# Kernel optimization log

Measured on AMD Instinct MI355X. Metric: run time of the kernel, lower is better.

Reference implementation:

```python
import jax, jax.numpy as jnp
import numpy as np

F, N, H = 1024, 16, 64  # features, num_heads, head_dim
B, T, S = 2, 1024, 2048  # batch, query len, memory (kv) len
M = S + 1                # relative position embeddings length


def _relative_shift(x):
    # x: [B, N, T, M] -> [B, N, T, M-1]  (Transformer-XL relative shift)
    b, h, q_len, k_len = x.shape
    x = jnp.pad(x, ((0, 0), (0, 0), (0, 0), (1, 0)))
    x = x.reshape(b, h, k_len + 1, q_len)
    x = x[:, :, 1:, :]
    x = x.reshape(b, h, q_len, k_len)
    return x[..., :-1]


def setup_inputs() -> dict:
    key = jax.random.key(0)
    ks = jax.random.split(key, 12)
    s = 1.0 / np.sqrt(F)
    return {
        'x': jax.random.normal(ks[0], (B, T, F), jnp.float32),
        'rel': jax.random.normal(ks[1], (M, F), jnp.float32),
        'memory': jax.random.normal(ks[2], (B, S, F), jnp.float32),
        'Wq': jax.random.normal(ks[3], (F, N, H), jnp.float32) * s,
        'Wk': jax.random.normal(ks[4], (F, N, H), jnp.float32) * s,
        'Wv': jax.random.normal(ks[5], (F, N, H), jnp.float32) * s,
        'Wr': jax.random.normal(ks[6], (F, N, H), jnp.float32) * s,
        'u_bias': jnp.zeros((N, H), jnp.float32),
        'v_bias': jnp.zeros((N, H), jnp.float32),
        'Wout': jax.random.normal(ks[7], (N * H, F), jnp.float32) * (1.0 / np.sqrt(N * H)),
        'b_out': jnp.zeros((F,), jnp.float32),
    }


def reference(x, rel, memory, Wq, Wk, Wv, Wr, u_bias, v_bias, Wout, b_out):
    b, t = x.shape[0], x.shape[1]
    # projections (DenseGeneral, no bias)
    q = jnp.einsum('btf,fnh->btnh', x, Wq)
    k = jnp.einsum('bsf,fnh->bsnh', memory, Wk)
    v = jnp.einsum('bsf,fnh->bsnh', memory, Wv)
    r = jnp.einsum('mf,fnh->mnh', rel, Wr)
    head_dim = q.shape[-1]
    scale = 1.0 / jnp.sqrt(jnp.asarray(head_dim, jnp.float32))
    q_u = q + u_bias[None, None]
    q_v = q + v_bias[None, None]
    # relative position bias, materialized at [B,N,T,M] then shifted
    bd = jnp.einsum('btnh,mnh->bntm', q_v, r)
    bd = _relative_shift(bd)                        # [B,N,T,S]
    bias = (bd * scale).astype(jnp.float32)
    # attention (dot_product_attention math), q/k/v in bf16 per source
    qb = q_u.astype(jnp.bfloat16)
    kb = k.astype(jnp.bfloat16)
    vb = v.astype(jnp.bfloat16)
    logits = jnp.einsum('btnh,bsnh->bnts', qb, kb).astype(jnp.float32) * scale + bias
    probs = jax.nn.softmax(logits, axis=-1)         # fp32 softmax
    out = jnp.einsum('bnts,bsnh->btnh', probs.astype(jnp.bfloat16), vb)
    out = out.astype(jnp.float32).reshape(b, t, -1)  # [B,T,N*H]
    return out @ Wout + b_out
```

## Files before the change

kernel.cpp:

```cpp
#include <hip/hip_runtime.h>
#include <cmath>

#define C_SCALE 0.18033688011112042f

typedef __attribute__((ext_vector_type(8))) short bf16x8;
typedef __attribute__((ext_vector_type(8))) _Float16 half8;
typedef __attribute__((ext_vector_type(4))) _Float16 half4;
typedef __attribute__((ext_vector_type(4))) float f32x4;
typedef __attribute__((ext_vector_type(4))) unsigned short us4;

__device__ inline unsigned short bf16_rne(float f) {
    unsigned u = __builtin_bit_cast(unsigned, f);
    u += 0x7fff + ((u >> 16) & 1);
    return (unsigned short)(u >> 16);
}

__device__ inline void lds_dma16(const _Float16* g, _Float16* l) {
    __builtin_amdgcn_global_load_lds(
        (__attribute__((address_space(1))) void*)(void*)g,
        (__attribute__((address_space(3))) void*)(void*)l, 16, 0, 0);
}

__global__ __launch_bounds__(256) void prep_kernel(
    const float* __restrict__ x, const float* __restrict__ mem,
    const float* __restrict__ rel,
    const float* __restrict__ s0, const float* __restrict__ s1,
    const float* __restrict__ s2, const float* __restrict__ s3,
    const float* __restrict__ s4,
    _Float16* __restrict__ x16, _Float16* __restrict__ mem16,
    _Float16* __restrict__ rel16,
    _Float16* __restrict__ d0, _Float16* __restrict__ d1,
    _Float16* __restrict__ d2, _Float16* __restrict__ d3,
    _Float16* __restrict__ d4)
{
    const int bx = blockIdx.x, tid = threadIdx.x;
    if (bx < 1280) {
        __shared__ _Float16 T[64][72];
        const int z = bx >> 8, rem = bx & 255;
        const float* src = z == 0 ? s0 : z == 1 ? s1 : z == 2 ? s2 : z == 3 ? s3 : s4;
        _Float16*    dst = z == 0 ? d0 : z == 1 ? d1 : z == 2 ? d2 : z == 3 ? d3 : d4;
        const int r0 = (rem & 15) * 64, c0 = (rem >> 4) * 64;
        const int r = tid >> 4, c4 = (tid & 15) * 4;
        #pragma unroll
        for (int rr = 0; rr < 64; rr += 16) {
            float4 v = *(const float4*)(src + (size_t)(r0 + r + rr) * 1024 + c0 + c4);
            T[c4 + 0][r + rr] = (_Float16)v.x;
            T[c4 + 1][r + rr] = (_Float16)v.y;
            T[c4 + 2][r + rr] = (_Float16)v.z;
            T[c4 + 3][r + rr] = (_Float16)v.w;
        }
        __syncthreads();
        const int orow = tid >> 2, seg = (tid & 3) * 16;
        half8 h0 = *(const half8*)&T[orow][seg];
        half8 h1 = *(const half8*)&T[orow][seg + 8];
        *(half8*)(dst + (size_t)(c0 + orow) * 1024 + r0 + seg)     = h0;
        *(half8*)(dst + (size_t)(c0 + orow) * 1024 + r0 + seg + 8) = h1;
    } else {
        size_t i = ((size_t)(bx - 1280) * 256 + tid) * 8;
        if (i >= 8389632ull) return;
        const float* src; _Float16* dst; size_t off;
        if (i < 2097152ull)      { src = x;   dst = x16;   off = i; }
        else if (i < 6291456ull) { src = mem; dst = mem16; off = i - 2097152ull; }
        else                     { src = rel; dst = rel16; off = i - 6291456ull; }
        float4 a = *(const float4*)(src + off);
        float4 b = *(const float4*)(src + off + 4);
        half8 h;
        h[0]=(_Float16)a.x; h[1]=(_Float16)a.y; h[2]=(_Float16)a.z; h[3]=(_Float16)a.w;
        h[4]=(_Float16)b.x; h[5]=(_Float16)b.y; h[6]=(_Float16)b.z; h[7]=(_Float16)b.w;
        *(half8*)(dst + off) = h;
    }
}

__global__ __launch_bounds__(256) void proj3_kernel(
    const _Float16* __restrict__ x16, const _Float16* __restrict__ mem16,
    const _Float16* __restrict__ rel16,
    const _Float16* __restrict__ Wqt, const _Float16* __restrict__ Wkt,
    const _Float16* __restrict__ Wvt, const _Float16* __restrict__ Wrt,
    const float* __restrict__ ub, const float* __restrict__ vb,
    unsigned short* __restrict__ qu, _Float16* __restrict__ qv,
    unsigned short* __restrict__ kb, unsigned short* __restrict__ vtb,
    _Float16* __restrict__ rb)
{
    alignas(16) __shared__ _Float16 As[128 * 64];
    alignas(16) __shared__ _Float16 Bs[128 * 64];
    const int tid = threadIdx.x;
    const int lane = tid & 63, w = tid >> 6, c = lane & 15, g = lane >> 4;
    const int bx = blockIdx.x, col0 = blockIdx.y * 128;

    int mode, row0, rowmax;
    const _Float16 *Ap, *Bp;
    if (bx < 16)      { mode = 0; row0 = bx * 128;        rowmax = 2047; Ap = x16;   Bp = Wqt; }
    else if (bx < 48) { mode = 1; row0 = (bx - 16) * 128; rowmax = 4095; Ap = mem16; Bp = Wkt; }
    else if (bx < 80) { mode = 2; row0 = (bx - 48) * 128; rowmax = 4095; Ap = mem16; Bp = Wvt; }
    else              { mode = 3; row0 = (bx - 80) * 128; rowmax = 2048; Ap = rel16; Bp = Wrt; }

    const int qr = (w & 1) * 64, qc = (w >> 1) * 64;
    const int srow = lane >> 3, phys = lane & 7;
    f32x4 acc[4][4] = {};

    for (int k0 = 0; k0 < 1024; k0 += 64) {
        #pragma unroll
        for (int q = 0; q < 4; q++) {
            int row = 32 * w + 8 * q + srow;
            int log = phys ^ (row & 7);
            int ar = row0 + row; if (ar > rowmax) ar = rowmax;
            lds_dma16(Ap + (size_t)ar * 1024 + k0 + log * 8, &As[(32 * w + 8 * q) * 64]);
            lds_dma16(Bp + (size_t)(col0 + row) * 1024 + k0 + log * 8, &Bs[(32 * w + 8 * q) * 64]);
        }
        __syncthreads();
        #pragma unroll
        for (int s = 0; s < 2; s++) {
            half8 af[4], bf[4];
            #pragma unroll
            for (int i = 0; i < 4; i++) {
                int row = qr + 16 * i + c;
                af[i] = *(const half8*)&As[row * 64 + ((4 * s + g) ^ (row & 7)) * 8];
            }
            #pragma unroll
            for (int j = 0; j < 4; j++) {
                int row = qc + 16 * j + c;
                bf[j] = *(const half8*)&Bs[row * 64 + ((4 * s + g) ^ (row & 7)) * 8];
            }
            #pragma unroll
            for (int i = 0; i < 4; i++)
                #pragma unroll
                for (int j = 0; j < 4; j++)
                    acc[i][j] = __builtin_amdgcn_mfma_f32_16x16x32_f16(af[i], bf[j], acc[i][j], 0, 0, 0);
        }
        __syncthreads();
    }

    #pragma unroll
    for (int i = 0; i < 4; i++) {
        #pragma unroll
        for (int j = 0; j < 4; j++) {
            const int cg = col0 + qc + 16 * j + c;
            const int rbase = row0 + qr + 16 * i + 4 * g;
            if (mode == 0) {
                float u = ub[cg], v = vb[cg];
                #pragma unroll
                for (int rg = 0; rg < 4; rg++) {
                    size_t o = (size_t)(rbase + rg) * 1024 + cg;
                    qu[o] = bf16_rne(acc[i][j][rg] + u);
                    qv[o] = (_Float16)((acc[i][j][rg] + v) * C_SCALE);
                }
            } else if (mode == 1) {
                #pragma unroll
                for (int rg = 0; rg < 4; rg++)
                    kb[(size_t)(rbase + rg) * 1024 + cg] = bf16_rne(acc[i][j][rg]);
            } else if (mode == 2) {
                us4 pk;
                #pragma unroll
                for (int rg = 0; rg < 4; rg++) pk[rg] = bf16_rne(acc[i][j][rg]);
                int b = rbase >> 11, s = rbase & 2047;
                *(us4*)&vtb[((size_t)(b * 16 + (cg >> 6)) * 64 + (cg & 63)) * 2048 + s] = pk;
            } else {
                #pragma unroll
                for (int rg = 0; rg < 4; rg++) {
                    int r_g = rbase + rg;
                    if (r_g < 2049)
                        rb[((size_t)(cg >> 6) * 2049 + r_g) * 64 + (cg & 63)] = (_Float16)acc[i][j][rg];
                }
            }
        }
    }
}

__global__ __launch_bounds__(256) void flash_kernel(
    const unsigned short* __restrict__ qu, const _Float16* __restrict__ qv,
    const unsigned short* __restrict__ kg, const unsigned short* __restrict__ vt,
    const _Float16* __restrict__ rb, _Float16* __restrict__ po, float* __restrict__ pl)
{
    __shared__ unsigned short Ks[64 * 70];
    __shared__ unsigned short Vs[64 * 70];
    __shared__ unsigned short PsT[64 * 70];
    __shared__ _Float16 BDX[64 * 138];
    const int tid = threadIdx.x;
    const int lane = tid & 63, w = tid >> 6, c = lane & 15, g = lane >> 4;
    const int id = blockIdx.x;
    const int p_pair = id & 127;
    const int t0 = (id >> 7) * 64;
    const int bn = p_pair >> 2, part = p_pair & 3;
    const int b = bn >> 4, n = bn & 15;
    const int s_start = part * 512;
    const int d0 = s_start - t0;

    const int tg = t0 + 16 * w + c;
    const unsigned short* qp = qu + (size_t)(b * 1024 + tg) * 1024 + n * 64 + g * 8;
    bf16x8 qf0 = *(const bf16x8*)qp;
    bf16x8 qf1 = *(const bf16x8*)(qp + 32);
    const _Float16* qvp = qv + (size_t)(b * 1024 + tg) * 1024 + n * 64 + g * 8;
    half8 av0 = *(const half8*)qvp;
    half8 av1 = *(const half8*)(qvp + 32);
    int tg2 = tg + 1; if (tg2 > 1023) tg2 = 1023;
    const _Float16* qvp2 = qv + (size_t)(b * 1024 + tg2) * 1024 + n * 64 + g * 8;
    half8 aw0 = *(const half8*)qvp2;
    half8 aw1 = *(const half8*)(qvp2 + 32);

    const _Float16* rbase = rb + (size_t)n * 2049 * 64;

    f32x4 o[4] = {};
    float l_acc = 0.f;

    const int myrow = (16 * w + c);

    auto bd_quad = [&](int Dbase) {
        #pragma unroll
        for (int i = 0; i < 4; i++) {
            const int Dmin = Dbase + 16 * i;
            const int Drow = Dmin + c;
            int mm = (Drow <= 1026) ? (Drow + 1023 > 2048 ? 2048 : Drow + 1023)
                                    : Drow - 1027;
            const _Float16* rp = rbase + (size_t)mm * 64 + g * 8;
            half8 r0 = *(const half8*)rp;
            half8 r1 = *(const half8*)(rp + 32);
            f32x4 z;
            if (Dmin + 15 <= 1026) {
                f32x4 zm = {};
                zm = __builtin_amdgcn_mfma_f32_16x16x32_f16(r0, av0, zm, 0, 0, 0);
                zm = __builtin_amdgcn_mfma_f32_16x16x32_f16(r1, av1, zm, 0, 0, 0);
                z = zm;
            } else if (Dmin >= 1027) {
                f32x4 zw = {};
                zw = __builtin_amdgcn_mfma_f32_16x16x32_f16(r0, aw0, zw, 0, 0, 0);
                zw = __builtin_amdgcn_mfma_f32_16x16x32_f16(r1, aw1, zw, 0, 0, 0);
                z = zw;
            } else {
                f32x4 zm = {}, zw = {};
                zm = __builtin_amdgcn_mfma_f32_16x16x32_f16(r0, av0, zm, 0, 0, 0);
                zm = __builtin_amdgcn_mfma_f32_16x16x32_f16(r1, av1, zm, 0, 0, 0);
                zw = __builtin_amdgcn_mfma_f32_16x16x32_f16(r0, aw0, zw, 0, 0, 0);
                zw = __builtin_amdgcn_mfma_f32_16x16x32_f16(r1, aw1, zw, 0, 0, 0);
                #pragma unroll
                for (int rg = 0; rg < 4; rg++)
                    z[rg] = (Dmin + 4 * g + rg >= 1027) ? zw[rg] : zm[rg];
            }
            int dz = 1026 - Dmin - 4 * g;
            if (dz >= 0 && dz < 4) z[dz] = 0.f;
            half4 hv;
            #pragma unroll
            for (int rg = 0; rg < 4; rg++) hv[rg] = (_Float16)z[rg];
            int slot0 = (Dmin + 4 * g - d0 + 63) & 127;
            _Float16* wp = &BDX[myrow * 138 + slot0];
            *(half4*)wp = hv;
            if (slot0 < 4) *(half4*)(wp + 128) = hv;
        }
    };

    bd_quad(d0 - 63);
    bd_quad(d0 + 1);

    const int sr = tid >> 2, scc = (tid & 3) * 16;
    const unsigned short* kst = kg + (size_t)(b * 2048 + s_start + sr) * 1024 + n * 64 + scc;
    const unsigned short* vst = vt + ((size_t)bn * 64 + sr) * 2048 + s_start + scc;

    for (int kk = 0; kk < 8; kk++) {
        const int diff0 = d0 + kk * 64;

        *(uint4*)&Ks[sr * 70 + scc]     = *(const uint4*)(kst + (size_t)(kk * 64) * 1024);
        *(uint4*)&Ks[sr * 70 + scc + 8] = *(const uint4*)(kst + (size_t)(kk * 64) * 1024 + 8);
        *(uint4*)&Vs[sr * 70 + scc]     = *(const uint4*)(vst + kk * 64);
        *(uint4*)&Vs[sr * 70 + scc + 8] = *(const uint4*)(vst + kk * 64 + 8);
        __syncthreads();

        #pragma unroll
        for (int i = 0; i < 4; i++) {
            bf16x8 kf0 = *(const bf16x8*)&Ks[(16 * i + c) * 70 + 8 * g];
            bf16x8 kf1 = *(const bf16x8*)&Ks[(16 * i + c) * 70 + 32 + 8 * g];
            f32x4 sa = {};
            sa = __builtin_amdgcn_mfma_f32_16x16x32_bf16(kf0, qf0, sa, 0, 0, 0);
            sa = __builtin_amdgcn_mfma_f32_16x16x32_bf16(kf1, qf1, sa, 0, 0, 0);
            int slotb = (64 * kk + 16 * i + 4 * g - myrow + 63) & 127;
            half4 bd4 = *(const half4*)&BDX[myrow * 138 + slotb];
            us4 pk;
            #pragma unroll
            for (int rg = 0; rg < 4; rg++) {
                float p = exp2f(fmaf(sa[rg], C_SCALE, (float)bd4[rg]));
                l_acc += p;
                pk[rg] = bf16_rne(p);
            }
            *(us4*)&PsT[myrow * 70 + 16 * i + 4 * g] = pk;
        }

        if (kk < 7) bd_quad(diff0 + 65);

        bf16x8 pf0 = *(const bf16x8*)&PsT[myrow * 70 + 8 * g];
        bf16x8 pf1 = *(const bf16x8*)&PsT[myrow * 70 + 32 + 8 * g];
        #pragma unroll
        for (int i2 = 0; i2 < 4; i2++) {
            bf16x8 vf0 = *(const bf16x8*)&Vs[(16 * i2 + c) * 70 + 8 * g];
            bf16x8 vf1 = *(const bf16x8*)&Vs[(16 * i2 + c) * 70 + 32 + 8 * g];
            o[i2] = __builtin_amdgcn_mfma_f32_16x16x32_bf16(vf0, pf0, o[i2], 0, 0, 0);
            o[i2] = __builtin_amdgcn_mfma_f32_16x16x32_bf16(vf1, pf1, o[i2], 0, 0, 0);
        }
        __syncthreads();
    }

    float s2 = l_acc;
    s2 += __shfl_xor(s2, 16);
    s2 += __shfl_xor(s2, 32);
    size_t rowb = ((size_t)part * 32 + bn) * 1024 + tg;
    if (g == 0) pl[rowb] = s2;
    float inv = 1.f / s2;
    #pragma unroll
    for (int i2 = 0; i2 < 4; i2++) {
        half4 hv;
        #pragma unroll
        for (int rg = 0; rg < 4; rg++) hv[rg] = (_Float16)(o[i2][rg] * inv);
        *(half4*)&po[rowb * 64 + 16 * i2 + 4 * g] = hv;
    }
}

__global__ __launch_bounds__(256) void combine_kernel(
    const _Float16* __restrict__ po, const float* __restrict__ pl,
    _Float16* __restrict__ attn)
{
    int f = blockIdx.x * 256 + threadIdx.x;
    int h = f & 63, t = (f >> 6) & 1023, bn = f >> 16;
    float os = 0.f, ls = 0.f;
    #pragma unroll
    for (int p = 0; p < 4; p++) {
        size_t rowb = ((size_t)p * 32 + bn) * 1024 + t;
        float lp = pl[rowb];
        os += lp * (float)po[rowb * 64 + h];
        ls += lp;
    }
    int b = bn >> 4, n = bn & 15;
    attn[((size_t)b * 1024 + t) * 1024 + n * 64 + h] = (_Float16)(os / ls);
}

__global__ __launch_bounds__(256) void out3_kernel(
    const _Float16* __restrict__ A, const _Float16* __restrict__ Bt,
    const float* __restrict__ bias, float* __restrict__ out)
{
    alignas(16) __shared__ _Float16 As[128 * 64];
    alignas(16) __shared__ _Float16 Bs[128 * 64];
    const int tid = threadIdx.x;
    const int lane = tid & 63, w = tid >> 6, c = lane & 15, g = lane >> 4;
    const int row0 = blockIdx.x * 128, col0 = blockIdx.y * 128;
    const int qr = (w & 1) * 64, qc = (w >> 1) * 64;
    const int srow = lane >> 3, phys = lane & 7;
    f32x4 acc[4][4] = {};

    for (int k0 = 0; k0 < 1024; k0 += 64) {
        #pragma unroll
        for (int q = 0; q < 4; q++) {
            int row = 32 * w + 8 * q + srow;
            int log = phys ^ (row & 7);
            lds_dma16(A  + (size_t)(row0 + row) * 1024 + k0 + log * 8, &As[(32 * w + 8 * q) * 64]);
            lds_dma16(Bt + (size_t)(col0 + row) * 1024 + k0 + log * 8, &Bs[(32 * w + 8 * q) * 64]);
        }
        __syncthreads();
        #pragma unroll
        for (int s = 0; s < 2; s++) {
            half8 af[4], bf[4];
            #pragma unroll
            for (int i = 0; i < 4; i++) {
                int row = qr + 16 * i + c;
                af[i] = *(const half8*)&As[row * 64 + ((4 * s + g) ^ (row & 7)) * 8];
            }
            #pragma unroll
            for (int j = 0; j < 4; j++) {
                int row = qc + 16 * j + c;
                bf[j] = *(const half8*)&Bs[row * 64 + ((4 * s + g) ^ (row & 7)) * 8];
            }
            #pragma unroll
            for (int i = 0; i < 4; i++)
                #pragma unroll
                for (int j = 0; j < 4; j++)
                    acc[i][j] = __builtin_amdgcn_mfma_f32_16x16x32_f16(af[i], bf[j], acc[i][j], 0, 0, 0);
        }
        __syncthreads();
    }
    #pragma unroll
    for (int i = 0; i < 4; i++)
        #pragma unroll
        for (int j = 0; j < 4; j++) {
            const int cg = col0 + qc + 16 * j + c;
            const int rbase = row0 + qr + 16 * i + 4 * g;
            #pragma unroll
            for (int rg = 0; rg < 4; rg++)
                out[(size_t)(rbase + rg) * 1024 + cg] = acc[i][j][rg] + bias[cg];
        }
}

extern "C" void kernel_launch(void* const* d_in, const int* in_sizes, int n_in,
                              void* d_out, int out_size, void* d_ws, size_t ws_size,
                              hipStream_t stream)
{
    const float* x    = (const float*)d_in[0];
    const float* rel  = (const float*)d_in[1];
    const float* mem  = (const float*)d_in[2];
    const float* Wq   = (const float*)d_in[3];
    const float* Wk   = (const float*)d_in[4];
    const float* Wv   = (const float*)d_in[5];
    const float* Wr   = (const float*)d_in[6];
    const float* ub   = (const float*)d_in[7];
    const float* vb   = (const float*)d_in[8];
    const float* Wout = (const float*)d_in[9];
    const float* bout = (const float*)d_in[10];
    float* out = (float*)d_out;

    char* ws = (char*)d_ws;
    unsigned short* qu    = (unsigned short*)(ws);
    _Float16*       qv    = (_Float16*)(ws + (4ull << 20));
    unsigned short* kb    = (unsigned short*)(ws + (8ull << 20));
    unsigned short* vtb   = (unsigned short*)(ws + (16ull << 20));
    _Float16*       rb    = (_Float16*)(ws + (24ull << 20));
    _Float16*       attn  = (_Float16*)(ws + (29ull << 20));
    _Float16*       po    = (_Float16*)(ws + (33ull << 20));
    float*          pl    = (float*)(ws + (50ull << 20));
    _Float16*       x16   = (_Float16*)(ws + (51ull << 20));
    _Float16*       mem16 = (_Float16*)(ws + (55ull << 20));
    _Float16*       rel16 = (_Float16*)(ws + (63ull << 20));
    _Float16*       Wqt   = (_Float16*)(ws + (68ull << 20));
    _Float16*       Wkt   = (_Float16*)(ws + (70ull << 20));
    _Float16*       Wvt   = (_Float16*)(ws + (72ull << 20));
    _Float16*       Wrt   = (_Float16*)(ws + (74ull << 20));
    _Float16*       Woutt = (_Float16*)(ws + (76ull << 20));

    prep_kernel<<<dim3(5377), 256, 0, stream>>>(
        x, mem, rel, Wq, Wk, Wv, Wr, Wout,
        x16, mem16, rel16, Wqt, Wkt, Wvt, Wrt, Woutt);
    proj3_kernel<<<dim3(97, 8), 256, 0, stream>>>(
        x16, mem16, rel16, Wqt, Wkt, Wvt, Wrt, ub, vb, qu, qv, kb, vtb, rb);
    flash_kernel<<<dim3(2048), 256, 0, stream>>>(qu, qv, kb, vtb, rb, po, pl);
    combine_kernel<<<dim3(8192), 256, 0, stream>>>(po, pl, attn);
    out3_kernel<<<dim3(16, 8), 256, 0, stream>>>(attn, Woutt, bout, out);
}
```

Baseline: 308.3 us.

## Stage K/V/R tiles via global_load_lds DMA with XOR swizzle, keep P in registers

The flash kernel now stages K, V and the relative-position rows R into LDS using global_load_lds DMA, with an XOR-swizzled unpadded layout in place of padded row strides. The BD computation reads R from LDS instead of directly from global memory. The P tile no longer makes a round trip through LDS: it stays in registers and feeds 16x16x16 bf16 MFMAs against V. This removes register-staged global loads and the PsT LDS traffic, at the cost of extra barriers and serialized staging with no double buffering.

```diff
diff --git a/kernel.cpp b/kernel.cpp
--- a/kernel.cpp
+++ b/kernel.cpp
@@ -4,6 +4,7 @@
 #define C_SCALE 0.18033688011112042f
 
 typedef __attribute__((ext_vector_type(8))) short bf16x8;
+typedef __attribute__((ext_vector_type(4))) short bf16x4;
 typedef __attribute__((ext_vector_type(8))) _Float16 half8;
 typedef __attribute__((ext_vector_type(4))) _Float16 half4;
 typedef __attribute__((ext_vector_type(4))) float f32x4;
@@ -15,7 +16,7 @@
     return (unsigned short)(u >> 16);
 }
 
-__device__ inline void lds_dma16(const _Float16* g, _Float16* l) {
+__device__ inline void lds_dma16(const void* g, void* l) {
     __builtin_amdgcn_global_load_lds(
         (__attribute__((address_space(1))) void*)(void*)g,
         (__attribute__((address_space(3))) void*)(void*)l, 16, 0, 0);
@@ -171,10 +172,10 @@
     const unsigned short* __restrict__ kg, const unsigned short* __restrict__ vt,
     const _Float16* __restrict__ rb, _Float16* __restrict__ po, float* __restrict__ pl)
 {
-    __shared__ unsigned short Ks[64 * 70];
-    __shared__ unsigned short Vs[64 * 70];
-    __shared__ unsigned short PsT[64 * 70];
-    __shared__ _Float16 BDX[64 * 138];
+    alignas(16) __shared__ unsigned short Ks[64 * 64];
+    alignas(16) __shared__ unsigned short Vs[64 * 64];
+    alignas(16) __shared__ _Float16 Rs[64 * 64];
+    alignas(16) __shared__ _Float16 BDX[64 * 132];
     const int tid = threadIdx.x;
     const int lane = tid & 63, w = tid >> 6, c = lane & 15, g = lane >> 4;
     const int id = blockIdx.x;
@@ -184,6 +185,7 @@
     const int b = bn >> 4, n = bn & 15;
     const int s_start = part * 512;
     const int d0 = s_start - t0;
+    const int cx = c & 7;
 
     const int tg = t0 + 16 * w + c;
     const unsigned short* qp = qu + (size_t)(b * 1024 + tg) * 1024 + n * 64 + g * 8;
@@ -197,23 +199,47 @@
     half8 aw0 = *(const half8*)qvp2;
     half8 aw1 = *(const half8*)(qvp2 + 32);
 
-    const _Float16* rbase = rb + (size_t)n * 2049 * 64;
-
     f32x4 o[4] = {};
     float l_acc = 0.f;
-
-    const int myrow = (16 * w + c);
+    const int myrow = 16 * w + c;
+
+    const int srow8 = lane >> 3;
+    const int slog  = (lane & 7) ^ srow8;
+
+    auto stage_k = [&](int kk) {
+        #pragma unroll
+        for (int iss = 0; iss < 2; iss++) {
+            int row = 16 * w + 8 * iss + srow8;
+            lds_dma16(kg + (size_t)(b * 2048 + s_start + kk * 64 + row) * 1024 + n * 64 + slog * 8,
+                      &Ks[(16 * w + 8 * iss) * 64]);
+        }
+    };
+    auto stage_v = [&](int kk) {
+        #pragma unroll
+        for (int iss = 0; iss < 2; iss++) {
+            int row = 16 * w + 8 * iss + srow8;
+            lds_dma16(vt + ((size_t)bn * 64 + row) * 2048 + s_start + kk * 64 + slog * 8,
+                      &Vs[(16 * w + 8 * iss) * 64]);
+        }
+    };
+    auto stage_r = [&](int winbase) {
+        #pragma unroll
+        for (int iss = 0; iss < 2; iss++) {
+            int row = 16 * w + 8 * iss + srow8;
+            int D = winbase + row;
+            int mm = (D <= 1026) ? (D + 1023 > 2048 ? 2048 : D + 1023) : D - 1027;
+            lds_dma16(rb + ((size_t)n * 2049 + mm) * 64 + slog * 8,
+                      &Rs[(16 * w + 8 * iss) * 64]);
+        }
+    };
 
     auto bd_quad = [&](int Dbase) {
         #pragma unroll
         for (int i = 0; i < 4; i++) {
+            const int lr = 16 * i + c;
+            half8 r0 = *(const half8*)&Rs[lr * 64 + ((g ^ cx) * 8)];
+            half8 r1 = *(const half8*)&Rs[lr * 64 + (((4 + g) ^ cx) * 8)];
             const int Dmin = Dbase + 16 * i;
-            const int Drow = Dmin + c;
-            int mm = (Drow <= 1026) ? (Drow + 1023 > 2048 ? 2048 : Drow + 1023)
-                                    : Drow - 1027;
-            const _Float16* rp = rbase + (size_t)mm * 64 + g * 8;
-            half8 r0 = *(const half8*)rp;
-            half8 r1 = *(const half8*)(rp + 32);
             f32x4 z;
             if (Dmin + 15 <= 1026) {
                 f32x4 zm = {};
@@ -241,59 +267,71 @@
             #pragma unroll
             for (int rg = 0; rg < 4; rg++) hv[rg] = (_Float16)z[rg];
             int slot0 = (Dmin + 4 * g - d0 + 63) & 127;
-            _Float16* wp = &BDX[myrow * 138 + slot0];
+            _Float16* wp = &BDX[myrow * 132 + slot0];
             *(half4*)wp = hv;
             if (slot0 < 4) *(half4*)(wp + 128) = hv;
         }
     };
 
+    stage_r(d0 - 63);
+    __syncthreads();
     bd_quad(d0 - 63);
+    __syncthreads();
+    stage_r(d0 + 1);
+    __syncthreads();
     bd_quad(d0 + 1);
-
-    const int sr = tid >> 2, scc = (tid & 3) * 16;
-    const unsigned short* kst = kg + (size_t)(b * 2048 + s_start + sr) * 1024 + n * 64 + scc;
-    const unsigned short* vst = vt + ((size_t)bn * 64 + sr) * 2048 + s_start + scc;
+    __syncthreads();
+    stage_k(0); stage_v(0); stage_r(d0 + 65);
+    __syncthreads();
 
     for (int kk = 0; kk < 8; kk++) {
         const int diff0 = d0 + kk * 64;
 
-        *(uint4*)&Ks[sr * 70 + scc]     = *(const uint4*)(kst + (size_t)(kk * 64) * 1024);
-        *(uint4*)&Ks[sr * 70 + scc + 8] = *(const uint4*)(kst + (size_t)(kk * 64) * 1024 + 8);
-        *(uint4*)&Vs[sr * 70 + scc]     = *(const uint4*)(vst + kk * 64);
-        *(uint4*)&Vs[sr * 70 + scc + 8] = *(const uint4*)(vst + kk * 64 + 8);
-        __syncthreads();
-
+        f32x4 sa[4];
         #pragma unroll
         for (int i = 0; i < 4; i++) {
-            bf16x8 kf0 = *(const bf16x8*)&Ks[(16 * i + c) * 70 + 8 * g];
-            bf16x8 kf1 = *(const bf16x8*)&Ks[(16 * i + c) * 70 + 32 + 8 * g];
-            f32x4 sa = {};
-            sa = __builtin_amdgcn_mfma_f32_16x16x32_bf16(kf0, qf0, sa, 0, 0, 0);
-            sa = __builtin_amdgcn_mfma_f32_16x16x32_bf16(kf1, qf1, sa, 0, 0, 0);
+            const int lr = 16 * i + c;
+            bf16x8 kf0 = *(const bf16x8*)&Ks[lr * 64 + ((g ^ cx) * 8)];
+            bf16x8 kf1 = *(const bf16x8*)&Ks[lr * 64 + (((4 + g) ^ cx) * 8)];
+            f32x4 s = {};
+            s = __builtin_amdgcn_mfma_f32_16x16x32_bf16(kf0, qf0, s, 0, 0, 0);
+            sa[i] = __builtin_amdgcn_mfma_f32_16x16x32_bf16(kf1, qf1, s, 0, 0, 0);
+        }
+
+        bf16x4 pk[4];
+        #pragma unroll
+        for (int i = 0; i < 4; i++) {
             int slotb = (64 * kk + 16 * i + 4 * g - myrow + 63) & 127;
-            half4 bd4 = *(const half4*)&BDX[myrow * 138 + slotb];
-            us4 pk;
+            half4 bd4 = *(const half4*)&BDX[myrow * 132 + slotb];
+            bf16x4 t;
             #pragma unroll
             for (int rg = 0; rg < 4; rg++) {
-                float p = exp2f(fmaf(sa[rg], C_SCALE, (float)bd4[rg]));
+                float p = exp2f(fmaf(sa[i][rg], C_SCALE, (float)bd4[rg]));
                 l_acc += p;
-                pk[rg] = bf16_rne(p);
-            }
-            *(us4*)&PsT[myrow * 70 + 16 * i + 4 * g] = pk;
+                t[rg] = (short)bf16_rne(p);
+            }
+            pk[i] = t;
         }
 
         if (kk < 7) bd_quad(diff0 + 65);
 
-        bf16x8 pf0 = *(const bf16x8*)&PsT[myrow * 70 + 8 * g];
-        bf16x8 pf1 = *(const bf16x8*)&PsT[myrow * 70 + 32 + 8 * g];
         #pragma unroll
         for (int i2 = 0; i2 < 4; i2++) {
-            bf16x8 vf0 = *(const bf16x8*)&Vs[(16 * i2 + c) * 70 + 8 * g];
-            bf16x8 vf1 = *(const bf16x8*)&Vs[(16 * i2 + c) * 70 + 32 + 8 * g];
-            o[i2] = __builtin_amdgcn_mfma_f32_16x16x32_bf16(vf0, pf0, o[i2], 0, 0, 0);
-            o[i2] = __builtin_amdgcn_mfma_f32_16x16x32_bf16(vf1, pf1, o[i2], 0, 0, 0);
-        }
-        __syncthreads();
+            const int vr = 16 * i2 + c;
+            #pragma unroll
+            for (int i = 0; i < 4; i++) {
+                int ch = (2 * i + (g >> 1)) ^ cx;
+                bf16x4 vf = *(const bf16x4*)&Vs[vr * 64 + ch * 8 + (g & 1) * 4];
+                o[i2] = __builtin_amdgcn_mfma_f32_16x16x16bf16_1k(vf, pk[i], o[i2], 0, 0, 0);
+            }
+        }
+
+        if (kk < 7) {
+            __syncthreads();
+            stage_k(kk + 1); stage_v(kk + 1);
+            if (kk < 6) stage_r(d0 + 64 * kk + 129);
+            __syncthreads();
+        }
     }
 
     float s2 = l_acc;
```

Result: faster. 283.9 us (-7.9%).
